# Kernel tuning notes

Hardware: AMD Instinct MI355X
Metric: run time of the kernel (lower is better)

The kernel has to match this reference:

```python
import jax, jax.numpy as jnp
import numpy as np

EPS = 1e-6   # param.eps
DT = 1e-2    # param.dt
DX = 1.0     # param.dx
DY = 1.0     # param.dy
N_PARAM = 1.0  # param.N


def _lap(c, dx=1.0, dy=1.0):
    # 5-point periodic Laplacian stencil on the last two dims
    return ((jnp.roll(c, 1, -1) + jnp.roll(c, -1, -1) - 2.0 * c) / (dx * dx)
            + (jnp.roll(c, 1, -2) + jnp.roll(c, -1, -2) - 2.0 * c) / (dy * dy))


def _log_with_mask(m, eps=EPS):
    # masked positions get constant eps -> zero gradient there, like torch masked_fill
    return jnp.log(jnp.where(m < eps, eps, m))


def setup_inputs() -> dict:
    key = jax.random.key(0)
    ks = jax.random.split(key, 12)
    B, H, W = 8, 1024, 1024
    inp = {
        "cv": jax.random.uniform(ks[0], (B, H, W), dtype=jnp.float32),
        "ci": jax.random.uniform(ks[1], (B, H, W), dtype=jnp.float32),
        "eta": jax.random.uniform(ks[2], (B, H, W), dtype=jnp.float32),
    }
    names = ["energy_v0", "energy_i0", "kBT0", "kappa_v0", "kappa_i0",
             "kappa_eta0", "diff_v0", "diff_i0", "L0"]
    for i, n in enumerate(names):
        inp[n] = jax.random.uniform(ks[3 + i], (1,), dtype=jnp.float32)
    return inp


def reference(cv, ci, eta, energy_v0, energy_i0, kBT0, kappa_v0, kappa_i0,
              kappa_eta0, diff_v0, diff_i0, L0):
    energy_v = jnp.abs(energy_v0) + 0.001
    energy_i = jnp.abs(energy_i0) + 0.001
    kBT = jnp.abs(kBT0) + 0.001
    kappa_v = jnp.abs(kappa_v0) + 0.001
    kappa_i = jnp.abs(kappa_i0) + 0.001
    kappa_eta = jnp.abs(kappa_eta0) + 0.001
    diff_v = jnp.abs(diff_v0) + 0.001
    diff_i = jnp.abs(diff_i0) + 0.001
    L = jnp.abs(L0) + 0.001

    lap_cv = _lap(cv, DX, DY)
    lap_ci = _lap(ci, DX, DY)
    lap_eta = _lap(eta, DX, DY)

    h = (eta - 1.0) ** 2
    j = eta ** 2
    cs = 1.0 - cv - ci
    log_cv = _log_with_mask(cv)
    log_ci = _log_with_mask(ci)
    log_cs = _log_with_mask(cs)

    fs = energy_v * cv + energy_i * ci + kBT * (cv * log_cv + ci * log_ci + cs * log_cs)
    dfs_dcv = energy_v + kBT * (log_cv - log_cs)
    dfs_dci = energy_i + kBT * (log_ci - log_cs)

    fv = (cv - 1.0) ** 2 + ci ** 2
    dfv_dcv = 2.0 * (cv - 1.0)
    dfv_dci = 2.0 * ci

    dF_dcv = h * dfs_dcv + j * dfv_dcv - kappa_v * lap_cv
    dF_dci = h * dfs_dci + j * dfv_dci - kappa_i * lap_ci
    dF_deta = N_PARAM * (fs * 2.0 * (eta - 1.0) + fv * 2.0 * eta - kappa_eta * lap_eta)

    mv = diff_v * cv / kBT
    mi = diff_i * ci / kBT

    cv_new = jnp.clip(cv + DT * (mv * _lap(dF_dcv)), 0.0, 1.0)
    ci_new = jnp.clip(ci + DT * (mi * _lap(dF_dci)), 0.0, 1.0)
    eta_new = jnp.clip(eta + DT * (-L * dF_deta), 0.0, 1.0)
    return cv_new, ci_new, eta_new
```

## Files before the change

kernel.cpp:

```cpp
#include <hip/hip_runtime.h>

#define WMASK 1023
#define LOG2W 10
#define HW (1024 * 1024)

#define EPS 1e-6f
#define DT 1e-2f

#define TX 64
#define TY 16
#define TPB 4

#define RST 72
#define NTASK 1044
#define RAWF (NTASK * 4)
#define CI_OFF 1440
#define ETA_OFF 2880
#define SST 64

typedef float f4 __attribute__((ext_vector_type(4)));
typedef unsigned int u32;

__device__ __forceinline__ float scal(const float* __restrict__ p) {
    return fabsf(p[0]) + 0.001f;
}
__device__ __forceinline__ float clip01(float v) {
    return fminf(fmaxf(v, 0.0f), 1.0f);
}
__device__ __forceinline__ float lg2m(float m) {
    return __log2f(fmaxf(m, EPS));
}

__device__ __forceinline__ void lgkm_barrier() {
    asm volatile("s_waitcnt lgkmcnt(0)" ::: "memory");
    __builtin_amdgcn_s_barrier();
}
__device__ __forceinline__ void vm_barrier() {
    asm volatile("s_waitcnt vmcnt(0)" ::: "memory");
    __builtin_amdgcn_s_barrier();
}

__device__ __forceinline__ void gld16(const float* g, float* l) {
    __builtin_amdgcn_global_load_lds(
        (const __attribute__((address_space(1))) u32*)g,
        (__attribute__((address_space(3))) u32*)l, 16, 0, 0);
}

__global__ __launch_bounds__(256, 3) void irr_fused(
    const float* __restrict__ cv,
    const float* __restrict__ ci,
    const float* __restrict__ eta,
    const float* __restrict__ p_ev,
    const float* __restrict__ p_ei,
    const float* __restrict__ p_kbt,
    const float* __restrict__ p_kv,
    const float* __restrict__ p_ki,
    const float* __restrict__ p_ke,
    const float* __restrict__ p_dv,
    const float* __restrict__ p_di,
    const float* __restrict__ p_L,
    float* __restrict__ cv_new,
    float* __restrict__ ci_new,
    float* __restrict__ eta_new)
{
    __shared__ __attribute__((aligned(16))) float sraw[2][RAWF];
    __shared__ __attribute__((aligned(16))) float sdv[16][SST];
    __shared__ __attribute__((aligned(16))) float sdi[16][SST];

    const int tid = threadIdx.x;
    const int x0 = blockIdx.x * TX;
    const int y0 = blockIdx.y * (TY * TPB);
    const int bbase = blockIdx.z * HW;

    const float energy_v = scal(p_ev);
    const float energy_i = scal(p_ei);
    const float kBT      = scal(p_kbt);
    const float kappa_v  = scal(p_kv);
    const float kappa_i  = scal(p_ki);
    const float kappa_e  = scal(p_ke);
    const float diff_v   = scal(p_dv);
    const float diff_i   = scal(p_di);
    const float L        = scal(p_L);
    const float kl   = kBT * 0.69314718056f;
    const float dtl  = DT * L;
    const float dtrv = DT * diff_v / kBT;
    const float dtri = DT * diff_i / kBT;

    const float* tsrc[5];
    int trow[5];
    #pragma unroll
    for (int i = 0; i < 5; ++i) {
        const int t = tid + (i << 8);
        if (i == 4 && tid >= NTASK - 1024) { tsrc[i] = cv; trow[i] = 0; continue; }
        const float* src; int r, ry0;
        if (t < 360)      { src = cv;  r = t;       ry0 = -2; }
        else if (t < 720) { src = ci;  r = t - 360; ry0 = -2; }
        else              { src = eta; r = t - 720; ry0 = -1; }
        const int cx = r % 18;
        const int cy = r / 18;
        tsrc[i] = src + bbase + ((x0 - 4 + (cx << 2)) & WMASK);
        trow[i] = ry0 + cy;
    }

    auto stage_async = [&](int b, int y0t) {
        #pragma unroll
        for (int i = 0; i < 5; ++i) {
            if (i < 4 || tid < NTASK - 1024) {
                const int gy = (trow[i] + y0t) & WMASK;
                gld16(tsrc[i] + (gy << LOG2W), &sraw[b][(tid + (i << 8)) << 2]);
            }
        }
    };

    int cur = 0;
    stage_async(0, y0);
    vm_barrier();

    const int k  = tid & 15;
    const int ey = tid >> 4;
    const int rx = (k << 2) + 4;
    const int c  = k << 2;

    for (int tl = 0; tl < TPB; ++tl) {
        const int y0t = y0 + tl * TY;

        if (tl + 1 < TPB) stage_async(cur ^ 1, y0 + (tl + 1) * TY);

        const f4 cC = *(const f4*)&sraw[cur][(ey + 2) * RST + rx];
        const f4 cU = *(const f4*)&sraw[cur][(ey + 1) * RST + rx];
        const f4 cD = *(const f4*)&sraw[cur][(ey + 3) * RST + rx];
        const f4 iC = *(const f4*)&sraw[cur][CI_OFF + (ey + 2) * RST + rx];
        const f4 iU = *(const f4*)&sraw[cur][CI_OFF + (ey + 1) * RST + rx];
        const f4 iD = *(const f4*)&sraw[cur][CI_OFF + (ey + 3) * RST + rx];
        const f4 eC = *(const f4*)&sraw[cur][ETA_OFF + (ey + 1) * RST + rx];
        const f4 eU = *(const f4*)&sraw[cur][ETA_OFF + (ey)     * RST + rx];
        const f4 eD = *(const f4*)&sraw[cur][ETA_OFF + (ey + 2) * RST + rx];

        float cL = __shfl_up(cC[3], 1), cR = __shfl_down(cC[0], 1);
        float iL = __shfl_up(iC[3], 1), iR = __shfl_down(iC[0], 1);
        float eL = __shfl_up(eC[3], 1), eR = __shfl_down(eC[0], 1);
        if (k == 0) {
            cL = sraw[cur][(ey + 2) * RST + 3];
            iL = sraw[cur][CI_OFF + (ey + 2) * RST + 3];
            eL = sraw[cur][ETA_OFF + (ey + 1) * RST + 3];
        }
        if (k == 15) {
            cR = sraw[cur][(ey + 2) * RST + 68];
            iR = sraw[cur][CI_OFF + (ey + 2) * RST + 68];
            eR = sraw[cur][ETA_OFF + (ey + 1) * RST + 68];
        }

        f4 dv, di, en;
        #pragma unroll
        for (int j = 0; j < 4; ++j) {
            const float c0 = cC[j];
            const float i0 = iC[j];
            const float e0 = eC[j];
            const float cl = (j == 0) ? cL : cC[j - 1];
            const float cr = (j == 3) ? cR : cC[j + 1];
            const float il = (j == 0) ? iL : iC[j - 1];
            const float ir = (j == 3) ? iR : iC[j + 1];
            const float el = (j == 0) ? eL : eC[j - 1];
            const float er = (j == 3) ? eR : eC[j + 1];

            const float lap_cv  = cl + cr + cU[j] + cD[j] - 4.0f * c0;
            const float lap_ci  = il + ir + iU[j] + iD[j] - 4.0f * i0;
            const float lap_eta = el + er + eU[j] + eD[j] - 4.0f * e0;

            const float h  = (e0 - 1.0f) * (e0 - 1.0f);
            const float jj = e0 * e0;
            const float cs = 1.0f - c0 - i0;
            const float lgv = lg2m(c0);
            const float lgi = lg2m(i0);
            const float lgs = lg2m(cs);

            dv[j] = h * (energy_v + kl * (lgv - lgs)) + jj * (2.0f * (c0 - 1.0f))
                  - kappa_v * lap_cv;
            di[j] = h * (energy_i + kl * (lgi - lgs)) + jj * (2.0f * i0)
                  - kappa_i * lap_ci;

            const float fs = energy_v * c0 + energy_i * i0
                           + kl * (c0 * lgv + i0 * lgi + cs * lgs);
            const float fv = (c0 - 1.0f) * (c0 - 1.0f) + i0 * i0;
            const float dF_deta = fs * 2.0f * (e0 - 1.0f) + fv * 2.0f * e0
                                - kappa_e * lap_eta;
            en[j] = clip01(fmaf(-dtl, dF_deta, e0));
        }

        *(f4*)&sdv[ey][c] = dv;
        *(f4*)&sdi[ey][c] = di;

        float vL = __shfl_up(dv[3], 1), vR = __shfl_down(dv[0], 1);
        float wL = __shfl_up(di[3], 1), wR = __shfl_down(di[0], 1);

        lgkm_barrier();

        auto evalpt = [&](int cr, int cc, int er) -> float2 {
            const float c0 = sraw[cur][cr * RST + cc];
            const float lap_cv = sraw[cur][cr * RST + cc - 1]
                               + sraw[cur][cr * RST + cc + 1]
                               + sraw[cur][(cr - 1) * RST + cc]
                               + sraw[cur][(cr + 1) * RST + cc] - 4.0f * c0;
            const float i0 = sraw[cur][CI_OFF + cr * RST + cc];
            const float lap_ci = sraw[cur][CI_OFF + cr * RST + cc - 1]
                               + sraw[cur][CI_OFF + cr * RST + cc + 1]
                               + sraw[cur][CI_OFF + (cr - 1) * RST + cc]
                               + sraw[cur][CI_OFF + (cr + 1) * RST + cc] - 4.0f * i0;
            const float e0 = sraw[cur][ETA_OFF + er * RST + cc];
            const float h  = (e0 - 1.0f) * (e0 - 1.0f);
            const float jj = e0 * e0;
            const float cs = 1.0f - c0 - i0;
            const float lgv = lg2m(c0);
            const float lgi = lg2m(i0);
            const float lgs = lg2m(cs);
            const float dvx = h * (energy_v + kl * (lgv - lgs))
                            + jj * (2.0f * (c0 - 1.0f)) - kappa_v * lap_cv;
            const float dix = h * (energy_i + kl * (lgi - lgs))
                            + jj * (2.0f * i0) - kappa_i * lap_ci;
            return make_float2(dvx, dix);
        };

        if (k == 0) {
            const float2 r = evalpt(ey + 2, 3, ey + 1);
            vL = r.x; wL = r.y;
        }
        if (k == 15) {
            const float2 r = evalpt(ey + 2, 68, ey + 1);
            vR = r.x; wR = r.y;
        }

        f4 vU, wU, vD, wD;
        if (ey == 0) {
            #pragma unroll
            for (int j = 0; j < 4; ++j) {
                const float2 r = evalpt(1, rx + j, 0);
                vU[j] = r.x; wU[j] = r.y;
            }
        } else {
            vU = *(const f4*)&sdv[ey - 1][c];
            wU = *(const f4*)&sdi[ey - 1][c];
        }
        if (ey == 15) {
            #pragma unroll
            for (int j = 0; j < 4; ++j) {
                const float2 r = evalpt(18, rx + j, 17);
                vD[j] = r.x; wD[j] = r.y;
            }
        } else {
            vD = *(const f4*)&sdv[ey + 1][c];
            wD = *(const f4*)&sdi[ey + 1][c];
        }

        const int gidx = bbase + ((y0t + ey) << LOG2W) + (x0 + c);
        f4 outv, outi;
        #pragma unroll
        for (int j = 0; j < 4; ++j) {
            const float lv = ((j == 0) ? vL : dv[j - 1]) + ((j == 3) ? vR : dv[j + 1])
                           + vU[j] + vD[j] - 4.0f * dv[j];
            const float li = ((j == 0) ? wL : di[j - 1]) + ((j == 3) ? wR : di[j + 1])
                           + wU[j] + wD[j] - 4.0f * di[j];
            outv[j] = clip01(fmaf(dtrv * cC[j], lv, cC[j]));
            outi[j] = clip01(fmaf(dtri * iC[j], li, iC[j]));
        }
        __builtin_nontemporal_store(en,   (f4*)(eta_new + gidx));
        __builtin_nontemporal_store(outv, (f4*)(cv_new + gidx));
        __builtin_nontemporal_store(outi, (f4*)(ci_new + gidx));

        if (tl + 1 < TPB) {
            vm_barrier();
            cur ^= 1;
        }
    }
}

extern "C" void kernel_launch(void* const* d_in, const int* in_sizes, int n_in,
                              void* d_out, int out_size, void* d_ws, size_t ws_size,
                              hipStream_t stream) {
    const float* cv  = (const float*)d_in[0];
    const float* ci  = (const float*)d_in[1];
    const float* eta = (const float*)d_in[2];
    const float* p_ev  = (const float*)d_in[3];
    const float* p_ei  = (const float*)d_in[4];
    const float* p_kbt = (const float*)d_in[5];
    const float* p_kv  = (const float*)d_in[6];
    const float* p_ki  = (const float*)d_in[7];
    const float* p_ke  = (const float*)d_in[8];
    const float* p_dv  = (const float*)d_in[9];
    const float* p_di  = (const float*)d_in[10];
    const float* p_L   = (const float*)d_in[11];

    const int N = in_sizes[0];

    float* out     = (float*)d_out;
    float* cv_new  = out;
    float* ci_new  = out + N;
    float* eta_new = out + 2 * N;

    const dim3 block(256);
    const dim3 grid(1024 / TX, 1024 / (TY * TPB), N / HW);

    irr_fused<<<grid, block, 0, stream>>>(cv, ci, eta, p_ev, p_ei, p_kbt,
                                          p_kv, p_ki, p_ke, p_dv, p_di, p_L,
                                          cv_new, ci_new, eta_new);
}
```

Measured before the change: 217.0 us.

## Drop double-buffered multi-tile loop for one tile per block with higher occupancy

Removes the per-block loop over four row tiles and its double-buffered async LDS staging. Each block now handles a single 64x16 tile with one shared buffer, and the grid is four times taller. The launch-bounds occupancy hint rises from 3 to 6 blocks per CU, so latency is hidden by concurrent blocks instead of explicit prefetch. The cost is more halo reloads and more per-block setup, such as the scalar parameter loads and address computation.

```diff
diff --git a/kernel.cpp b/kernel.cpp
--- a/kernel.cpp
+++ b/kernel.cpp
@@ -9,7 +9,6 @@
 
 #define TX 64
 #define TY 16
-#define TPB 4
 
 #define RST 72
 #define NTASK 1044
@@ -46,7 +45,7 @@
         (__attribute__((address_space(3))) u32*)l, 16, 0, 0);
 }
 
-__global__ __launch_bounds__(256, 3) void irr_fused(
+__global__ __launch_bounds__(256, 6) void irr_fused(
     const float* __restrict__ cv,
     const float* __restrict__ ci,
     const float* __restrict__ eta,
@@ -63,14 +62,30 @@
     float* __restrict__ ci_new,
     float* __restrict__ eta_new)
 {
-    __shared__ __attribute__((aligned(16))) float sraw[2][RAWF];
+    __shared__ __attribute__((aligned(16))) float sraw[RAWF];
     __shared__ __attribute__((aligned(16))) float sdv[16][SST];
     __shared__ __attribute__((aligned(16))) float sdi[16][SST];
 
     const int tid = threadIdx.x;
     const int x0 = blockIdx.x * TX;
-    const int y0 = blockIdx.y * (TY * TPB);
+    const int y0 = blockIdx.y * TY;
     const int bbase = blockIdx.z * HW;
+
+    #pragma unroll
+    for (int i = 0; i < 5; ++i) {
+        const int t = tid + (i << 8);
+        if (i < 4 || tid < NTASK - 1024) {
+            const float* src; int r, ry0;
+            if (t < 360)      { src = cv;  r = t;       ry0 = y0 - 2; }
+            else if (t < 720) { src = ci;  r = t - 360; ry0 = y0 - 2; }
+            else              { src = eta; r = t - 720; ry0 = y0 - 1; }
+            const int cx = r % 18;
+            const int cy = r / 18;
+            const int gx = (x0 - 4 + (cx << 2)) & WMASK;
+            const int gy = (ry0 + cy) & WMASK;
+            gld16(src + bbase + (gy << LOG2W) + gx, &sraw[t << 2]);
+        }
+    }
 
     const float energy_v = scal(p_ev);
     const float energy_i = scal(p_ei);
@@ -86,34 +101,6 @@
     const float dtrv = DT * diff_v / kBT;
     const float dtri = DT * diff_i / kBT;
 
-    const float* tsrc[5];
-    int trow[5];
-    #pragma unroll
-    for (int i = 0; i < 5; ++i) {
-        const int t = tid + (i << 8);
-        if (i == 4 && tid >= NTASK - 1024) { tsrc[i] = cv; trow[i] = 0; continue; }
-        const float* src; int r, ry0;
-        if (t < 360)      { src = cv;  r = t;       ry0 = -2; }
-        else if (t < 720) { src = ci;  r = t - 360; ry0 = -2; }
-        else              { src = eta; r = t - 720; ry0 = -1; }
-        const int cx = r % 18;
-        const int cy = r / 18;
-        tsrc[i] = src + bbase + ((x0 - 4 + (cx << 2)) & WMASK);
-        trow[i] = ry0 + cy;
-    }
-
-    auto stage_async = [&](int b, int y0t) {
-        #pragma unroll
-        for (int i = 0; i < 5; ++i) {
-            if (i < 4 || tid < NTASK - 1024) {
-                const int gy = (trow[i] + y0t) & WMASK;
-                gld16(tsrc[i] + (gy << LOG2W), &sraw[b][(tid + (i << 8)) << 2]);
-            }
-        }
-    };
-
-    int cur = 0;
-    stage_async(0, y0);
     vm_barrier();
 
     const int k  = tid & 15;
@@ -121,156 +108,145 @@
     const int rx = (k << 2) + 4;
     const int c  = k << 2;
 
-    for (int tl = 0; tl < TPB; ++tl) {
-        const int y0t = y0 + tl * TY;
-
-        if (tl + 1 < TPB) stage_async(cur ^ 1, y0 + (tl + 1) * TY);
-
-        const f4 cC = *(const f4*)&sraw[cur][(ey + 2) * RST + rx];
-        const f4 cU = *(const f4*)&sraw[cur][(ey + 1) * RST + rx];
-        const f4 cD = *(const f4*)&sraw[cur][(ey + 3) * RST + rx];
-        const f4 iC = *(const f4*)&sraw[cur][CI_OFF + (ey + 2) * RST + rx];
-        const f4 iU = *(const f4*)&sraw[cur][CI_OFF + (ey + 1) * RST + rx];
-        const f4 iD = *(const f4*)&sraw[cur][CI_OFF + (ey + 3) * RST + rx];
-        const f4 eC = *(const f4*)&sraw[cur][ETA_OFF + (ey + 1) * RST + rx];
-        const f4 eU = *(const f4*)&sraw[cur][ETA_OFF + (ey)     * RST + rx];
-        const f4 eD = *(const f4*)&sraw[cur][ETA_OFF + (ey + 2) * RST + rx];
-
-        float cL = __shfl_up(cC[3], 1), cR = __shfl_down(cC[0], 1);
-        float iL = __shfl_up(iC[3], 1), iR = __shfl_down(iC[0], 1);
-        float eL = __shfl_up(eC[3], 1), eR = __shfl_down(eC[0], 1);
-        if (k == 0) {
-            cL = sraw[cur][(ey + 2) * RST + 3];
-            iL = sraw[cur][CI_OFF + (ey + 2) * RST + 3];
-            eL = sraw[cur][ETA_OFF + (ey + 1) * RST + 3];
-        }
-        if (k == 15) {
-            cR = sraw[cur][(ey + 2) * RST + 68];
-            iR = sraw[cur][CI_OFF + (ey + 2) * RST + 68];
-            eR = sraw[cur][ETA_OFF + (ey + 1) * RST + 68];
-        }
-
-        f4 dv, di, en;
+    const f4 cC = *(const f4*)&sraw[(ey + 2) * RST + rx];
+    const f4 cU = *(const f4*)&sraw[(ey + 1) * RST + rx];
+    const f4 cD = *(const f4*)&sraw[(ey + 3) * RST + rx];
+    const f4 iC = *(const f4*)&sraw[CI_OFF + (ey + 2) * RST + rx];
+    const f4 iU = *(const f4*)&sraw[CI_OFF + (ey + 1) * RST + rx];
+    const f4 iD = *(const f4*)&sraw[CI_OFF + (ey + 3) * RST + rx];
+    const f4 eC = *(const f4*)&sraw[ETA_OFF + (ey + 1) * RST + rx];
+    const f4 eU = *(const f4*)&sraw[ETA_OFF + (ey)     * RST + rx];
+    const f4 eD = *(const f4*)&sraw[ETA_OFF + (ey + 2) * RST + rx];
+
+    float cL = __shfl_up(cC[3], 1), cR = __shfl_down(cC[0], 1);
+    float iL = __shfl_up(iC[3], 1), iR = __shfl_down(iC[0], 1);
+    float eL = __shfl_up(eC[3], 1), eR = __shfl_down(eC[0], 1);
+    if (k == 0) {
+        cL = sraw[(ey + 2) * RST + 3];
+        iL = sraw[CI_OFF + (ey + 2) * RST + 3];
+        eL = sraw[ETA_OFF + (ey + 1) * RST + 3];
+    }
+    if (k == 15) {
+        cR = sraw[(ey + 2) * RST + 68];
+        iR = sraw[CI_OFF + (ey + 2) * RST + 68];
+        eR = sraw[ETA_OFF + (ey + 1) * RST + 68];
+    }
+
+    f4 dv, di, en;
+    #pragma unroll
+    for (int j = 0; j < 4; ++j) {
+        const float c0 = cC[j];
+        const float i0 = iC[j];
+        const float e0 = eC[j];
+        const float cl = (j == 0) ? cL : cC[j - 1];
+        const float cr = (j == 3) ? cR : cC[j + 1];
+        const float il = (j == 0) ? iL : iC[j - 1];
+        const float ir = (j == 3) ? iR : iC[j + 1];
+        const float el = (j == 0) ? eL : eC[j - 1];
+        const float er = (j == 3) ? eR : eC[j + 1];
+
+        const float lap_cv  = cl + cr + cU[j] + cD[j] - 4.0f * c0;
+        const float lap_ci  = il + ir + iU[j] + iD[j] - 4.0f * i0;
+        const float lap_eta = el + er + eU[j] + eD[j] - 4.0f * e0;
+
+        const float h  = (e0 - 1.0f) * (e0 - 1.0f);
+        const float jj = e0 * e0;
+        const float cs = 1.0f - c0 - i0;
+        const float lgv = lg2m(c0);
+        const float lgi = lg2m(i0);
+        const float lgs = lg2m(cs);
+
+        dv[j] = h * (energy_v + kl * (lgv - lgs)) + jj * (2.0f * (c0 - 1.0f))
+              - kappa_v * lap_cv;
+        di[j] = h * (energy_i + kl * (lgi - lgs)) + jj * (2.0f * i0)
+              - kappa_i * lap_ci;
+
+        const float fs = energy_v * c0 + energy_i * i0
+                       + kl * (c0 * lgv + i0 * lgi + cs * lgs);
+        const float fv = (c0 - 1.0f) * (c0 - 1.0f) + i0 * i0;
+        const float dF_deta = fs * 2.0f * (e0 - 1.0f) + fv * 2.0f * e0
+                            - kappa_e * lap_eta;
+        en[j] = clip01(fmaf(-dtl, dF_deta, e0));
+    }
+
+    *(f4*)&sdv[ey][c] = dv;
+    *(f4*)&sdi[ey][c] = di;
+
+    float vL = __shfl_up(dv[3], 1), vR = __shfl_down(dv[0], 1);
+    float wL = __shfl_up(di[3], 1), wR = __shfl_down(di[0], 1);
+
+    lgkm_barrier();
+
+    auto evalpt = [&](int cr, int cc, int er) -> float2 {
+        const float c0 = sraw[cr * RST + cc];
+        const float lap_cv = sraw[cr * RST + cc - 1]
+                           + sraw[cr * RST + cc + 1]
+                           + sraw[(cr - 1) * RST + cc]
+                           + sraw[(cr + 1) * RST + cc] - 4.0f * c0;
+        const float i0 = sraw[CI_OFF + cr * RST + cc];
+        const float lap_ci = sraw[CI_OFF + cr * RST + cc - 1]
+                           + sraw[CI_OFF + cr * RST + cc + 1]
+                           + sraw[CI_OFF + (cr - 1) * RST + cc]
+                           + sraw[CI_OFF + (cr + 1) * RST + cc] - 4.0f * i0;
+        const float e0 = sraw[ETA_OFF + er * RST + cc];
+        const float h  = (e0 - 1.0f) * (e0 - 1.0f);
+        const float jj = e0 * e0;
+        const float cs = 1.0f - c0 - i0;
+        const float lgv = lg2m(c0);
+        const float lgi = lg2m(i0);
+        const float lgs = lg2m(cs);
+        const float dvx = h * (energy_v + kl * (lgv - lgs))
+                        + jj * (2.0f * (c0 - 1.0f)) - kappa_v * lap_cv;
+        const float dix = h * (energy_i + kl * (lgi - lgs))
+                        + jj * (2.0f * i0) - kappa_i * lap_ci;
+        return make_float2(dvx, dix);
+    };
+
+    if (k == 0) {
+        const float2 r = evalpt(ey + 2, 3, ey + 1);
+        vL = r.x; wL = r.y;
+    }
+    if (k == 15) {
+        const float2 r = evalpt(ey + 2, 68, ey + 1);
+        vR = r.x; wR = r.y;
+    }
+
+    f4 vU, wU, vD, wD;
+    if (ey == 0) {
         #pragma unroll
         for (int j = 0; j < 4; ++j) {
-            const float c0 = cC[j];
-            const float i0 = iC[j];
-            const float e0 = eC[j];
-            const float cl = (j == 0) ? cL : cC[j - 1];
-            const float cr = (j == 3) ? cR : cC[j + 1];
-            const float il = (j == 0) ? iL : iC[j - 1];
-            const float ir = (j == 3) ? iR : iC[j + 1];
-            const float el = (j == 0) ? eL : eC[j - 1];
-            const float er = (j == 3) ? eR : eC[j + 1];
-
-            const float lap_cv  = cl + cr + cU[j] + cD[j] - 4.0f * c0;
-            const float lap_ci  = il + ir + iU[j] + iD[j] - 4.0f * i0;
-            const float lap_eta = el + er + eU[j] + eD[j] - 4.0f * e0;
-
-            const float h  = (e0 - 1.0f) * (e0 - 1.0f);
-            const float jj = e0 * e0;
-            const float cs = 1.0f - c0 - i0;
-            const float lgv = lg2m(c0);
-            const float lgi = lg2m(i0);
-            const float lgs = lg2m(cs);
-
-            dv[j] = h * (energy_v + kl * (lgv - lgs)) + jj * (2.0f * (c0 - 1.0f))
-                  - kappa_v * lap_cv;
-            di[j] = h * (energy_i + kl * (lgi - lgs)) + jj * (2.0f * i0)
-                  - kappa_i * lap_ci;
-
-            const float fs = energy_v * c0 + energy_i * i0
-                           + kl * (c0 * lgv + i0 * lgi + cs * lgs);
-            const float fv = (c0 - 1.0f) * (c0 - 1.0f) + i0 * i0;
-            const float dF_deta = fs * 2.0f * (e0 - 1.0f) + fv * 2.0f * e0
-                                - kappa_e * lap_eta;
-            en[j] = clip01(fmaf(-dtl, dF_deta, e0));
+            const float2 r = evalpt(1, rx + j, 0);
+            vU[j] = r.x; wU[j] = r.y;
         }
-
-        *(f4*)&sdv[ey][c] = dv;
-        *(f4*)&sdi[ey][c] = di;
-
-        float vL = __shfl_up(dv[3], 1), vR = __shfl_down(dv[0], 1);
-        float wL = __shfl_up(di[3], 1), wR = __shfl_down(di[0], 1);
-
-        lgkm_barrier();
-
-        auto evalpt = [&](int cr, int cc, int er) -> float2 {
-            const float c0 = sraw[cur][cr * RST + cc];
-            const float lap_cv = sraw[cur][cr * RST + cc - 1]
-                               + sraw[cur][cr * RST + cc + 1]
-                               + sraw[cur][(cr - 1) * RST + cc]
-                               + sraw[cur][(cr + 1) * RST + cc] - 4.0f * c0;
-            const float i0 = sraw[cur][CI_OFF + cr * RST + cc];
-            const float lap_ci = sraw[cur][CI_OFF + cr * RST + cc - 1]
-                               + sraw[cur][CI_OFF + cr * RST + cc + 1]
-                               + sraw[cur][CI_OFF + (cr - 1) * RST + cc]
-                               + sraw[cur][CI_OFF + (cr + 1) * RST + cc] - 4.0f * i0;
-            const float e0 = sraw[cur][ETA_OFF + er * RST + cc];
-            const float h  = (e0 - 1.0f) * (e0 - 1.0f);
-            const float jj = e0 * e0;
-            const float cs = 1.0f - c0 - i0;
-            const float lgv = lg2m(c0);
-            const float lgi = lg2m(i0);
-            const float lgs = lg2m(cs);
-            const float dvx = h * (energy_v + kl * (lgv - lgs))
-                            + jj * (2.0f * (c0 - 1.0f)) - kappa_v * lap_cv;
-            const float dix = h * (energy_i + kl * (lgi - lgs))
-                            + jj * (2.0f * i0) - kappa_i * lap_ci;
-            return make_float2(dvx, dix);
-        };
-
-        if (k == 0) {
-            const float2 r = evalpt(ey + 2, 3, ey + 1);
-            vL = r.x; wL = r.y;
-        }
-        if (k == 15) {
-            const float2 r = evalpt(ey + 2, 68, ey + 1);
-            vR = r.x; wR = r.y;
-        }
-
-        f4 vU, wU, vD, wD;
-        if (ey == 0) {
-            #pragma unroll
-            for (int j = 0; j < 4; ++j) {
-                const float2 r = evalpt(1, rx + j, 0);
-                vU[j] = r.x; wU[j] = r.y;
-            }
-        } else {
-            vU = *(const f4*)&sdv[ey - 1][c];
-            wU = *(const f4*)&sdi[ey - 1][c];
-        }
-        if (ey == 15) {
-            #pragma unroll
-            for (int j = 0; j < 4; ++j) {
-                const float2 r = evalpt(18, rx + j, 17);
-                vD[j] = r.x; wD[j] = r.y;
-            }
-        } else {
-            vD = *(const f4*)&sdv[ey + 1][c];
-            wD = *(const f4*)&sdi[ey + 1][c];
-        }
-
-        const int gidx = bbase + ((y0t + ey) << LOG2W) + (x0 + c);
-        f4 outv, outi;
+    } else {
+        vU = *(const f4*)&sdv[ey - 1][c];
+        wU = *(const f4*)&sdi[ey - 1][c];
+    }
+    if (ey == 15) {
         #pragma unroll
         for (int j = 0; j < 4; ++j) {
-            const float lv = ((j == 0) ? vL : dv[j - 1]) + ((j == 3) ? vR : dv[j + 1])
-                           + vU[j] + vD[j] - 4.0f * dv[j];
-            const float li = ((j == 0) ? wL : di[j - 1]) + ((j == 3) ? wR : di[j + 1])
-                           + wU[j] + wD[j] - 4.0f * di[j];
-            outv[j] = clip01(fmaf(dtrv * cC[j], lv, cC[j]));
-            outi[j] = clip01(fmaf(dtri * iC[j], li, iC[j]));
+            const float2 r = evalpt(18, rx + j, 17);
+            vD[j] = r.x; wD[j] = r.y;
         }
-        __builtin_nontemporal_store(en,   (f4*)(eta_new + gidx));
-        __builtin_nontemporal_store(outv, (f4*)(cv_new + gidx));
-        __builtin_nontemporal_store(outi, (f4*)(ci_new + gidx));
-
-        if (tl + 1 < TPB) {
-            vm_barrier();
-            cur ^= 1;
-        }
-    }
+    } else {
+        vD = *(const f4*)&sdv[ey + 1][c];
+        wD = *(const f4*)&sdi[ey + 1][c];
+    }
+
+    const int gidx = bbase + ((y0 + ey) << LOG2W) + (x0 + c);
+    f4 outv, outi;
+    #pragma unroll
+    for (int j = 0; j < 4; ++j) {
+        const float lv = ((j == 0) ? vL : dv[j - 1]) + ((j == 3) ? vR : dv[j + 1])
+                       + vU[j] + vD[j] - 4.0f * dv[j];
+        const float li = ((j == 0) ? wL : di[j - 1]) + ((j == 3) ? wR : di[j + 1])
+                       + wU[j] + wD[j] - 4.0f * di[j];
+        outv[j] = clip01(fmaf(dtrv * cC[j], lv, cC[j]));
+        outi[j] = clip01(fmaf(dtri * iC[j], li, iC[j]));
+    }
+    __builtin_nontemporal_store(en,   (f4*)(eta_new + gidx));
+    __builtin_nontemporal_store(outv, (f4*)(cv_new + gidx));
+    __builtin_nontemporal_store(outi, (f4*)(ci_new + gidx));
 }
 
 extern "C" void kernel_launch(void* const* d_in, const int* in_sizes, int n_in,
@@ -297,7 +273,7 @@
     float* eta_new = out + 2 * N;
 
     const dim3 block(256);
-    const dim3 grid(1024 / TX, 1024 / (TY * TPB), N / HW);
+    const dim3 grid(1024 / TX, 1024 / TY, N / HW);
 
     irr_fused<<<grid, block, 0, stream>>>(cv, ci, eta, p_ev, p_ei, p_kbt,
                                           p_kv, p_ki, p_ke, p_dv, p_di, p_L,
```

Result: slower. 320.3 us (+47.6%).
